# Optimization experiments

Measured on AMD Instinct MI355X. Metric: run time of the kernel, lower is better.

The kernel has to match this reference:

```python
import jax, jax.numpy as jnp
import numpy as np

N_NODES = 65536   # N
D_HID   = 128     # D (hidden)
N_GROUPS = 16384  # G portfolios
GROUP_LEN = 64    # lines per portfolio (port_len entries)
N_LINES = N_GROUPS * GROUP_LEN  # L
BATCH = 16384     # B samples


def setup_inputs() -> dict:
    key = jax.random.key(0)
    k = jax.random.split(key, 5)
    H = jax.random.normal(k[0], (N_NODES, D_HID), dtype=jnp.float32)
    port_w_signed_flat = jax.random.normal(k[1], (N_LINES,), dtype=jnp.float32)
    anchor_idx = jax.random.randint(k[2], (BATCH,), 0, N_NODES, dtype=jnp.int32)
    pf_gid = jax.random.randint(k[3], (BATCH,), 0, N_GROUPS, dtype=jnp.int32)
    port_nodes_flat = jax.random.randint(k[4], (N_LINES,), 0, N_NODES, dtype=jnp.int32)
    port_len = jnp.full((N_GROUPS,), GROUP_LEN, dtype=jnp.int32)
    return {
        'H': H,
        'port_w_signed_flat': port_w_signed_flat,
        'anchor_idx': anchor_idx,
        'pf_gid': pf_gid,
        'port_nodes_flat': port_nodes_flat,
        'port_len': port_len,
    }


def reference(H, port_w_signed_flat, anchor_idx, pf_gid, port_nodes_flat, port_len):
    """Faithful, vectorized port of compute_samplewise_portfolio_vectors_loo.

    Ragged segment-weighted mean per portfolio group, with strict leave-one-out
    correction for each sample's anchor node, followed by L2 normalization.
    Returns (V_abs, V_sgn), each [B, D].
    """
    N, D = H.shape
    G = port_len.shape[0]
    L = port_nodes_flat.shape[0]

    # gid per flat line: repeat_interleave(arange(G), lens)
    gid_lines = jnp.repeat(jnp.arange(G, dtype=jnp.int32), port_len,
                           total_repeat_length=L)

    w_abs = jnp.abs(port_w_signed_flat)
    Hl = H[port_nodes_flat]                                  # [L, D] gather
    S_abs = jax.ops.segment_sum(w_abs[:, None] * Hl, gid_lines, num_segments=G)
    W_abs = jax.ops.segment_sum(w_abs, gid_lines, num_segments=G)
    W_sgn = jax.ops.segment_sum(port_w_signed_flat, gid_lines, num_segments=G)

    valid = (pf_gid >= 0) & (pf_gid < G)
    g = jnp.clip(pf_gid, 0, G - 1)

    # Leave-one-out self-weight: sum of w over lines where (gid==g_i, node==anchor_i).
    # Vectorized join via a sorted composite int32 key (G*N < 2^31 by construction).
    keys_l = gid_lines * N + port_nodes_flat                 # [L]
    keys_s = g * N + anchor_idx                              # [B]
    order = jnp.argsort(keys_l)
    sk = keys_l[order]
    zero1 = jnp.zeros((1,), H.dtype)
    ca = jnp.concatenate([zero1, jnp.cumsum(w_abs[order])])
    cs = jnp.concatenate([zero1, jnp.cumsum(port_w_signed_flat[order])])
    lo = jnp.searchsorted(sk, keys_s, side='left')
    hi = jnp.searchsorted(sk, keys_s, side='right')
    self_w_abs = ca[hi] - ca[lo]                             # [B]
    self_w_sgn = cs[hi] - cs[lo]                             # [B]

    Ha = H[anchor_idx]                                       # [B, D]
    denom = jnp.maximum(W_abs[g] - self_w_abs, 1e-12)        # clamp_min
    V_abs = (S_abs[g] - self_w_abs[:, None] * Ha) / denom[:, None]
    V_sgn = ((W_sgn[g] - self_w_sgn) / denom)[:, None] * V_abs

    V_abs = jnp.where(valid[:, None], V_abs, jnp.zeros((), H.dtype))
    V_sgn = jnp.where(valid[:, None], V_sgn, jnp.zeros((), H.dtype))

    # torch F.normalize: x / clamp(||x||, min=eps)
    na = jnp.linalg.norm(V_abs, axis=1, keepdims=True)
    V_abs = V_abs / jnp.maximum(na, 1e-6)
    ns = jnp.linalg.norm(V_sgn, axis=1, keepdims=True)
    V_sgn = jnp.where(ns > 0, V_sgn / jnp.maximum(ns, 1e-6), V_sgn)
    return V_abs, V_sgn
```

## Files before the change

kernel.cpp:

```cpp
#include <hip/hip_runtime.h>
#include <hip/hip_bf16.h>


#define DDIM 128

__device__ inline unsigned bf_rne(float x) {
    unsigned u = __float_as_uint(x);
    return (u + 0x7FFFu + ((u >> 16) & 1u)) >> 16;
}

__device__ inline void unpack2(unsigned d, float& lo, float& hi) {
    lo = __uint_as_float(d << 16);
    hi = __uint_as_float(d & 0xFFFF0000u);
}

__global__ __launch_bounds__(1024) void init_kernel(
    const float4* __restrict__ H4, uint2* __restrict__ Hb, int n4, int N,
    const int* __restrict__ plen, int* __restrict__ offs, int G,
    const int* __restrict__ pf_gid, int* __restrict__ used, int B, int nconv) {
    const int t = threadIdx.x;
    const int bb = blockIdx.x;
    if (bb < nconv) {
        const int i = bb * 1024 + t;
        if (i < n4) {
            const float4 v = H4[i];
            uint2 o;
            o.x = bf_rne(v.x) | (bf_rne(v.y) << 16);
            o.y = bf_rne(v.z) | (bf_rne(v.w) << 16);
            const int n = i >> 5;
            const int j = i & 31;
            const int p = j >> 3;
            const int k = j & 7;
            Hb[(size_t)p * ((size_t)N * 8) + (size_t)n * 8 + k] = o;
        }
        return;
    }
    if (bb == nconv) {
        for (int i = t; i < G; i += 1024) used[i] = 0;
        __syncthreads();
        for (int i = t; i < B; i += 1024) {
            const int g = pf_gid[i];
            if (g >= 0 && g < G) used[g] = 1;
        }
        return;
    }
    __shared__ int part[1024];
    const int chunk = (G + 1023) >> 10;
    const int lo = min(t * chunk, G);
    const int hi = min(lo + chunk, G);
    int s = 0;
    for (int i = lo; i < hi; ++i) s += plen[i];
    part[t] = s;
    __syncthreads();
    #pragma unroll
    for (int ofs = 1; ofs < 1024; ofs <<= 1) {
        int v = (t >= ofs) ? part[t - ofs] : 0;
        __syncthreads();
        part[t] += v;
        __syncthreads();
    }
    int run = part[t] - s;
    for (int i = lo; i < hi; ++i) { offs[i] = run; run += plen[i]; }
}

__global__ __launch_bounds__(256) void group_sums(
    const unsigned short* __restrict__ Hp,
    const float* __restrict__ pw, const int* __restrict__ pn,
    const int* __restrict__ plen, const int* __restrict__ offs,
    const int* __restrict__ used,
    float* __restrict__ Sabs, float* __restrict__ Wag,
    float* __restrict__ Wsg, int G, int N) {
    const int b = blockIdx.x;
    const int slot = b & 7;
    const int p = slot & 3;
    const int wid = threadIdx.x >> 6;
    const int g = (b >> 3) * 8 + (slot >> 2) * 4 + wid;
    if (g >= G) return;
    if (!used[g]) return;
    const int lane = threadIdx.x & 63;

    __shared__ unsigned char tile[4][4096];

    const unsigned short* plane = Hp + (size_t)p * ((size_t)N * 32);
    const int off = offs[g];
    const int len = plen[g];

    const int sg = lane & 3;
    const int s8 = lane & 7;
    float acc0 = 0.f, acc1 = 0.f, acc2 = 0.f, acc3 = 0.f;
    float laWa = 0.f, laWs = 0.f;

    for (int base = 0; base < len; base += 64) {
        asm volatile("s_waitcnt lgkmcnt(0)" ::: "memory");

        float wl = 0.f;
        int nl = 0;
        if (base + lane < len) {
            wl = pw[off + base + lane];
            nl = pn[off + base + lane];
        }
        laWa += fabsf(wl);
        laWs += wl;

        #pragma unroll
        for (int it = 0; it < 4; ++it) {
            const int row = __shfl(nl, it * 16 + (lane >> 2));
            const unsigned short* gp = plane + (size_t)row * 32 + sg * 8;
            __builtin_amdgcn_global_load_lds(
                (const __attribute__((address_space(1))) unsigned int*)gp,
                (__attribute__((address_space(3))) unsigned int*)&tile[wid][it * 1024],
                16, 0, 0);
        }
        asm volatile("s_waitcnt vmcnt(0)" ::: "memory");

        #pragma unroll
        for (int j = 0; j < 8; ++j) {
            const int row = j * 8 + (lane >> 3);
            const float ww = fabsf(__shfl(wl, row));
            const uint2 hv = *(const uint2*)&tile[wid][row * 64 + s8 * 8];
            float f0, f1, f2, f3;
            unpack2(hv.x, f0, f1);
            unpack2(hv.y, f2, f3);
            acc0 = fmaf(ww, f0, acc0);
            acc1 = fmaf(ww, f1, acc1);
            acc2 = fmaf(ww, f2, acc2);
            acc3 = fmaf(ww, f3, acc3);
        }
    }

    #pragma unroll
    for (int m = 8; m < 64; m <<= 1) {
        acc0 += __shfl_xor(acc0, m);
        acc1 += __shfl_xor(acc1, m);
        acc2 += __shfl_xor(acc2, m);
        acc3 += __shfl_xor(acc3, m);
    }
    if (lane < 8) {
        float4* dst = (float4*)(Sabs + (size_t)g * DDIM + p * 32 + 4 * lane);
        *dst = make_float4(acc0, acc1, acc2, acc3);
    }
    if (p == 0) {
        #pragma unroll
        for (int m = 32; m; m >>= 1) {
            laWa += __shfl_xor(laWa, m);
            laWs += __shfl_xor(laWs, m);
        }
        if (lane == 0) { Wag[g] = laWa; Wsg[g] = laWs; }
    }
}

__global__ __launch_bounds__(256) void per_sample(
    const unsigned short* __restrict__ Hp,
    const float* __restrict__ pw, const int* __restrict__ pn,
    const int* __restrict__ plen, const int* __restrict__ offs,
    const float* __restrict__ Sabs, const float* __restrict__ Wag,
    const float* __restrict__ Wsg,
    const int* __restrict__ anchor_idx, const int* __restrict__ pf_gid,
    float* __restrict__ out, int B, int G, int N) {
    const int b = blockIdx.x * (blockDim.x >> 6) + (threadIdx.x >> 6);
    const int lane = threadIdx.x & 63;
    if (b >= B) return;

    float2* outA = (float2*)(out + (size_t)b * DDIM);
    float2* outS = (float2*)(out + ((size_t)B + b) * DDIM);

    const int g = pf_gid[b];
    if (!(g >= 0 && g < G)) {
        const float2 z = make_float2(0.f, 0.f);
        outA[lane] = z;
        outS[lane] = z;
        return;
    }

    const int anchor = anchor_idx[b];
    const int off = offs[g];
    const int len = plen[g];

    float selfa = 0.f, selfs = 0.f;
    for (int base = 0; base < len; base += 64) {
        const int jmax = min(64, len - base);
        if (lane < jmax) {
            const float w = pw[off + base + lane];
            const int n = pn[off + base + lane];
            if (n == anchor) { selfa += fabsf(w); selfs += w; }
        }
    }
    #pragma unroll
    for (int m = 32; m; m >>= 1) {
        selfa += __shfl_xor(selfa, m);
        selfs += __shfl_xor(selfs, m);
    }

    const float Wa = Wag[g];
    const float Wsn = Wsg[g];
    const float2 S = ((const float2*)(Sabs + (size_t)g * DDIM))[lane];
    const unsigned hb = *(const unsigned*)(Hp + (size_t)(lane >> 4) * ((size_t)N * 32)
                                              + (size_t)anchor * 32 + (lane & 15) * 2);
    float h0, h1;
    unpack2(hb, h0, h1);

    const float denom = fmaxf(Wa - selfa, 1e-12f);
    float2 v;
    v.x = (S.x - selfa * h0) / denom;
    v.y = (S.y - selfa * h1) / denom;
    const float scale = (Wsn - selfs) / denom;

    float n2 = v.x * v.x + v.y * v.y;
    #pragma unroll
    for (int m = 32; m; m >>= 1) n2 += __shfl_xor(n2, m);
    const float na = sqrtf(n2);

    const float invA = 1.0f / fmaxf(na, 1e-6f);
    const float ns = fabsf(scale) * na;
    const float sgnscale = (ns > 0.f) ? (scale / fmaxf(ns, 1e-6f)) : scale;

    outA[lane] = make_float2(v.x * invA, v.y * invA);
    outS[lane] = make_float2(v.x * sgnscale, v.y * sgnscale);
}

__global__ __launch_bounds__(1024) void scan_only(
    const int* __restrict__ len, int* __restrict__ offs, int G) {
    __shared__ int part[1024];
    const int t = threadIdx.x;
    const int chunk = (G + 1023) >> 10;
    const int lo = min(t * chunk, G);
    const int hi = min(lo + chunk, G);
    int s = 0;
    for (int i = lo; i < hi; ++i) s += len[i];
    part[t] = s;
    __syncthreads();
    #pragma unroll
    for (int ofs = 1; ofs < 1024; ofs <<= 1) {
        int v = (t >= ofs) ? part[t - ofs] : 0;
        __syncthreads();
        part[t] += v;
        __syncthreads();
    }
    int run = part[t] - s;
    for (int i = lo; i < hi; ++i) { offs[i] = run; run += len[i]; }
}

__global__ __launch_bounds__(256) void pf_loo_f32(
    const float* __restrict__ H, const float* __restrict__ pw,
    const int* __restrict__ anchor_idx, const int* __restrict__ pf_gid,
    const int* __restrict__ pn, const int* __restrict__ plen,
    const int* __restrict__ offs, float* __restrict__ out, int B, int G) {
    const int b = blockIdx.x * (blockDim.x >> 6) + (threadIdx.x >> 6);
    const int lane = threadIdx.x & 63;
    const int half = lane >> 5;
    const int qlane = lane & 31;
    if (b >= B) return;
    float4* outA = (float4*)(out + (size_t)b * DDIM);
    float4* outS = (float4*)(out + ((size_t)B + b) * DDIM);
    const int gid = pf_gid[b];
    if (!(gid >= 0 && gid < G)) {
        float4 z = make_float4(0.f, 0.f, 0.f, 0.f);
        if (half == 0) { outA[qlane] = z; outS[qlane] = z; }
        return;
    }
    const int anchor = anchor_idx[b];
    const int off = offs[gid];
    const int len = plen[gid];
    float4 acc = make_float4(0.f, 0.f, 0.f, 0.f);
    float laWa = 0.f, laWs = 0.f, laSa = 0.f, laSs = 0.f;
    for (int base = 0; base < len; base += 64) {
        const int jmax = min(64, len - base);
        float wl = 0.f;
        int nl = -1;
        if (lane < jmax) { wl = pw[off + base + lane]; nl = pn[off + base + lane]; }
        const float wla = fabsf(wl);
        laWa += wla; laWs += wl;
        if (nl == anchor) { laSa += wla; laSs += wl; }
        #pragma unroll 8
        for (int jj = 0; jj < 64; jj += 2) {
            const float ww = fabsf(__shfl(wl, jj + half));
            const int row = __shfl(nl, jj + half);
            const float4 h = ((const float4*)(H + (size_t)row * DDIM))[qlane];
            acc.x = fmaf(ww, h.x, acc.x);
            acc.y = fmaf(ww, h.y, acc.y);
            acc.z = fmaf(ww, h.z, acc.z);
            acc.w = fmaf(ww, h.w, acc.w);
        }
    }
    #pragma unroll
    for (int m = 32; m; m >>= 1) {
        laWa += __shfl_xor(laWa, m);
        laWs += __shfl_xor(laWs, m);
        laSa += __shfl_xor(laSa, m);
        laSs += __shfl_xor(laSs, m);
    }
    acc.x += __shfl_xor(acc.x, 32);
    acc.y += __shfl_xor(acc.y, 32);
    acc.z += __shfl_xor(acc.z, 32);
    acc.w += __shfl_xor(acc.w, 32);
    const float denom = fmaxf(laWa - laSa, 1e-12f);
    const float4 hv = ((const float4*)(H + (size_t)anchor * DDIM))[qlane];
    float4 v;
    v.x = (acc.x - laSa * hv.x) / denom;
    v.y = (acc.y - laSa * hv.y) / denom;
    v.z = (acc.z - laSa * hv.z) / denom;
    v.w = (acc.w - laSa * hv.w) / denom;
    const float scale = (laWs - laSs) / denom;
    float n2 = v.x * v.x + v.y * v.y + v.z * v.z + v.w * v.w;
    #pragma unroll
    for (int m = 32; m; m >>= 1) n2 += __shfl_xor(n2, m);
    n2 *= 0.5f;
    const float na = sqrtf(n2);
    const float invA = 1.0f / fmaxf(na, 1e-6f);
    const float ns = fabsf(scale) * na;
    const float sgnscale = (ns > 0.f) ? (scale / fmaxf(ns, 1e-6f)) : scale;
    const float sc = half ? sgnscale : invA;
    float4 res = make_float4(v.x * sc, v.y * sc, v.z * sc, v.w * sc);
    float4* dst = half ? outS : outA;
    dst[qlane] = res;
}

extern "C" void kernel_launch(void* const* d_in, const int* in_sizes, int n_in,
                              void* d_out, int out_size, void* d_ws, size_t ws_size,
                              hipStream_t stream) {
    const float* H      = (const float*)d_in[0];
    const float* pw     = (const float*)d_in[1];
    const int* anchor   = (const int*)d_in[2];
    const int* gid      = (const int*)d_in[3];
    const int* pn       = (const int*)d_in[4];
    const int* plen     = (const int*)d_in[5];
    float* out          = (float*)d_out;

    const int B = in_sizes[2];
    const int G = in_sizes[5];
    const int ND = in_sizes[0];
    const int N  = ND / DDIM;
    const size_t hb_bytes = (size_t)ND * 2;
    const size_t sabs_bytes = (size_t)G * DDIM * 4;
    const size_t need = hb_bytes + sabs_bytes + (size_t)G * 4 * 4;

    if (ws_size >= need) {
        char* p = (char*)d_ws;
        unsigned short* Hb = (unsigned short*)p;        p += hb_bytes;
        float* Sabs        = (float*)p;                 p += sabs_bytes;
        int* offsp         = (int*)p;                   p += (size_t)G * 4;
        int* usedp         = (int*)p;                   p += (size_t)G * 4;
        float* Wag         = (float*)p;                 p += (size_t)G * 4;
        float* Wsg         = (float*)p;

        const int n4 = ND / 4;
        const int nconv = (n4 + 1023) / 1024;
        init_kernel<<<nconv + 2, 1024, 0, stream>>>(
            (const float4*)H, (uint2*)Hb, n4, N, plen, offsp, G, gid, usedp, B, nconv);

        const int gblocks = ((G + 7) / 8) * 8;
        group_sums<<<gblocks, 256, 0, stream>>>(Hb, pw, pn, plen, offsp, usedp,
                                                Sabs, Wag, Wsg, G, N);

        const int sblocks = (B + 3) / 4;
        per_sample<<<sblocks, 256, 0, stream>>>(Hb, pw, pn, plen, offsp, Sabs,
                                                Wag, Wsg, anchor, gid, out, B, G, N);
    } else {
        int* offsp = (int*)d_ws;
        scan_only<<<1, 1024, 0, stream>>>(plen, offsp, G);
        const int blocks = (B + 3) / 4;
        pf_loo_f32<<<blocks, 256, 0, stream>>>(H, pw, anchor, gid, pn, plen,
                                               offsp, out, B, G);
    }
}
```

Measured before the change: 146.3 us.

## Make group_sums persistent with prefetch and direct 16-byte gathers

The group_sums kernel becomes a grid-stride persistent kernel with the grid capped at 2048 blocks. Each wave prefetches the next group's offset, length, used flag, weights and node indices while it processes the current group. The LDS staging through global_load_lds is replaced by direct 16-byte global loads of bf16 rows, so each lane accumulates 8 features instead of 4. This is meant to cut launch and tail overhead, hide metadata load latency, and drop the LDS round-trip and waitcnt barriers, at the cost of more registers and fewer resident blocks.

```diff
diff --git a/kernel.cpp b/kernel.cpp
--- a/kernel.cpp
+++ b/kernel.cpp
@@ -73,79 +73,100 @@
     const int b = blockIdx.x;
     const int slot = b & 7;
     const int p = slot & 3;
+    const int h = slot >> 2;
     const int wid = threadIdx.x >> 6;
-    const int g = (b >> 3) * 8 + (slot >> 2) * 4 + wid;
-    if (g >= G) return;
-    if (!used[g]) return;
     const int lane = threadIdx.x & 63;
-
-    __shared__ unsigned char tile[4][4096];
-
+    const int sector = lane & 3;
+    const int rslot = lane >> 2;
     const unsigned short* plane = Hp + (size_t)p * ((size_t)N * 32);
-    const int off = offs[g];
-    const int len = plen[g];
-
-    const int sg = lane & 3;
-    const int s8 = lane & 7;
-    float acc0 = 0.f, acc1 = 0.f, acc2 = 0.f, acc3 = 0.f;
-    float laWa = 0.f, laWs = 0.f;
-
-    for (int base = 0; base < len; base += 64) {
-        asm volatile("s_waitcnt lgkmcnt(0)" ::: "memory");
-
-        float wl = 0.f;
-        int nl = 0;
-        if (base + lane < len) {
-            wl = pw[off + base + lane];
-            nl = pn[off + base + lane];
-        }
-        laWa += fabsf(wl);
-        laWs += wl;
-
-        #pragma unroll
-        for (int it = 0; it < 4; ++it) {
-            const int row = __shfl(nl, it * 16 + (lane >> 2));
-            const unsigned short* gp = plane + (size_t)row * 32 + sg * 8;
-            __builtin_amdgcn_global_load_lds(
-                (const __attribute__((address_space(1))) unsigned int*)gp,
-                (__attribute__((address_space(3))) unsigned int*)&tile[wid][it * 1024],
-                16, 0, 0);
-        }
-        asm volatile("s_waitcnt vmcnt(0)" ::: "memory");
-
-        #pragma unroll
-        for (int j = 0; j < 8; ++j) {
-            const int row = j * 8 + (lane >> 3);
-            const float ww = fabsf(__shfl(wl, row));
-            const uint2 hv = *(const uint2*)&tile[wid][row * 64 + s8 * 8];
-            float f0, f1, f2, f3;
-            unpack2(hv.x, f0, f1);
-            unpack2(hv.y, f2, f3);
-            acc0 = fmaf(ww, f0, acc0);
-            acc1 = fmaf(ww, f1, acc1);
-            acc2 = fmaf(ww, f2, acc2);
-            acc3 = fmaf(ww, f3, acc3);
-        }
-    }
-
-    #pragma unroll
-    for (int m = 8; m < 64; m <<= 1) {
-        acc0 += __shfl_xor(acc0, m);
-        acc1 += __shfl_xor(acc1, m);
-        acc2 += __shfl_xor(acc2, m);
-        acc3 += __shfl_xor(acc3, m);
-    }
-    if (lane < 8) {
-        float4* dst = (float4*)(Sabs + (size_t)g * DDIM + p * 32 + 4 * lane);
-        *dst = make_float4(acc0, acc1, acc2, acc3);
-    }
-    if (p == 0) {
-        #pragma unroll
-        for (int m = 32; m; m >>= 1) {
-            laWa += __shfl_xor(laWa, m);
-            laWs += __shfl_xor(laWs, m);
-        }
-        if (lane == 0) { Wag[g] = laWa; Wsg[g] = laWs; }
+    const int gstep = gridDim.x;
+
+    int g = (b >> 3) * 8 + h * 4 + wid;
+
+    float wl = 0.f; int nl = 0;
+    int off_c = 0, len_c = 0, used_c = 0;
+    if (g < G) {
+        off_c = offs[g]; len_c = plen[g]; used_c = used[g];
+        if (lane < len_c) { wl = pw[off_c + lane]; nl = pn[off_c + lane]; }
+    }
+
+    while (g < G) {
+        const int gn = g + gstep;
+        float wl_n = 0.f; int nl_n = 0;
+        int off_n = 0, len_n = 0, used_n = 0;
+        if (gn < G) {
+            off_n = offs[gn]; len_n = plen[gn]; used_n = used[gn];
+            if (lane < len_n) { wl_n = pw[off_n + lane]; nl_n = pn[off_n + lane]; }
+        }
+
+        if (used_c) {
+            float acc0 = 0.f, acc1 = 0.f, acc2 = 0.f, acc3 = 0.f;
+            float acc4 = 0.f, acc5 = 0.f, acc6 = 0.f, acc7 = 0.f;
+            float gWa = 0.f, gWs = 0.f;
+
+            float twl = wl; int tnl = nl;
+            int base = 0;
+            for (;;) {
+                gWa += fabsf(twl);
+                gWs += twl;
+                #pragma unroll
+                for (int it = 0; it < 4; ++it) {
+                    const int src = it * 16 + rslot;
+                    const float ww = fabsf(__shfl(twl, src));
+                    const int row = __shfl(tnl, src);
+                    const uint4 hv = *(const uint4*)(plane + (size_t)row * 32 + sector * 8);
+                    float f0, f1, f2, f3, f4, f5, f6, f7;
+                    unpack2(hv.x, f0, f1);
+                    unpack2(hv.y, f2, f3);
+                    unpack2(hv.z, f4, f5);
+                    unpack2(hv.w, f6, f7);
+                    acc0 = fmaf(ww, f0, acc0);
+                    acc1 = fmaf(ww, f1, acc1);
+                    acc2 = fmaf(ww, f2, acc2);
+                    acc3 = fmaf(ww, f3, acc3);
+                    acc4 = fmaf(ww, f4, acc4);
+                    acc5 = fmaf(ww, f5, acc5);
+                    acc6 = fmaf(ww, f6, acc6);
+                    acc7 = fmaf(ww, f7, acc7);
+                }
+                base += 64;
+                if (base >= len_c) break;
+                twl = 0.f; tnl = 0;
+                if (base + lane < len_c) {
+                    twl = pw[off_c + base + lane];
+                    tnl = pn[off_c + base + lane];
+                }
+            }
+
+            #pragma unroll
+            for (int m = 4; m < 64; m <<= 1) {
+                acc0 += __shfl_xor(acc0, m);
+                acc1 += __shfl_xor(acc1, m);
+                acc2 += __shfl_xor(acc2, m);
+                acc3 += __shfl_xor(acc3, m);
+                acc4 += __shfl_xor(acc4, m);
+                acc5 += __shfl_xor(acc5, m);
+                acc6 += __shfl_xor(acc6, m);
+                acc7 += __shfl_xor(acc7, m);
+            }
+            if (lane < 4) {
+                float4* dst = (float4*)(Sabs + (size_t)g * DDIM + p * 32 + 8 * lane);
+                dst[0] = make_float4(acc0, acc1, acc2, acc3);
+                dst[1] = make_float4(acc4, acc5, acc6, acc7);
+            }
+            if (p == 0) {
+                #pragma unroll
+                for (int m = 32; m; m >>= 1) {
+                    gWa += __shfl_xor(gWa, m);
+                    gWs += __shfl_xor(gWs, m);
+                }
+                if (lane == 0) { Wag[g] = gWa; Wsg[g] = gWs; }
+            }
+        }
+
+        g = gn;
+        wl = wl_n; nl = nl_n;
+        off_c = off_n; len_c = len_n; used_c = used_n;
     }
 }
 
@@ -348,7 +369,8 @@
         init_kernel<<<nconv + 2, 1024, 0, stream>>>(
             (const float4*)H, (uint2*)Hb, n4, N, plen, offsp, G, gid, usedp, B, nconv);
 
-        const int gblocks = ((G + 7) / 8) * 8;
+        int gblocks = ((G + 7) / 8) * 8;
+        if (gblocks > 2048) gblocks = 2048;
         group_sums<<<gblocks, 256, 0, stream>>>(Hb, pw, pn, plen, offsp, usedp,
                                                 Sabs, Wag, Wsg, G, N);
 
```

Measured after the change: 154.1 us. +5.3%, slower.
